# Kernel tuning notes

Hardware: AMD Instinct MI355X
Metric: run time of the kernel (lower is better)

Reference implementation:

```python
import jax, jax.numpy as jnp
import numpy as np
from jax import lax

B, T, H = 128, 8192, 96


def setup_inputs() -> dict:
    key = jax.random.key(0)
    ks = jax.random.split(key, 7)
    s = 1.0 / np.sqrt(H)  # PyTorch LSTM init scale
    return {
        "x": jax.random.normal(ks[0], (B, T, 1), dtype=jnp.float32),
        "w_ih": jax.random.uniform(ks[1], (4 * H, 1), jnp.float32, -s, s),
        "w_hh": jax.random.uniform(ks[2], (4 * H, H), jnp.float32, -s, s),
        "b_ih": jax.random.uniform(ks[3], (4 * H,), jnp.float32, -s, s),
        "b_hh": jax.random.uniform(ks[4], (4 * H,), jnp.float32, -s, s),
        "w_out": jax.random.uniform(ks[5], (1, H), jnp.float32, -s, s),
        "b_out": jax.random.uniform(ks[6], (1,), jnp.float32, -s, s),
    }


def reference(x, w_ih, w_hh, b_ih, b_hh, w_out, b_out):
    # x: [B, T, 1]; single-layer batch_first LSTM, zero initial (h, c).
    Bb, Tt, _ = x.shape
    Hh = w_hh.shape[1]
    # Precompute input contribution to all gates: [T, B, 4H]
    xg = jnp.einsum("bti,gi->btg", x, w_ih) + b_ih + b_hh
    xg = jnp.transpose(xg, (1, 0, 2))

    def step(carry, g):
        h, c = carry
        gates = g + h @ w_hh.T  # [B, 4H]
        i, f, gg, o = jnp.split(gates, 4, axis=-1)  # PyTorch order: i, f, g, o
        i = jax.nn.sigmoid(i)
        f = jax.nn.sigmoid(f)
        gg = jnp.tanh(gg)
        o = jax.nn.sigmoid(o)
        c = f * c + i * gg
        h = o * jnp.tanh(c)
        return (h, c), h

    h0 = jnp.zeros((Bb, Hh), x.dtype)
    (_, _), hs = lax.scan(step, (h0, h0), xg)  # hs: [T, B, H]
    hs = jnp.transpose(hs, (1, 0, 2))  # [B, T, H]
    return hs @ w_out.T + b_out  # [B, T, 1]
```

## Files before the change

### kernel.cpp

```cpp
#include <hip/hip_runtime.h>


#define T_LEN 8192
#define H_DIM 96
#define NTHR  256
#define CHUNK 128
#define LOG2E 1.44269504f

typedef float    f32x4 __attribute__((ext_vector_type(4)));
typedef _Float16 half8 __attribute__((ext_vector_type(8)));

#define MFMA16(A, B, C)                                                        \
    __builtin_amdgcn_mfma_f32_16x16x32_f16(__builtin_bit_cast(half8, (A)),     \
                                           __builtin_bit_cast(half8, (B)),     \
                                           (C), 0, 0, 0)

__device__ __forceinline__ float sig2(float s) {
    return __builtin_amdgcn_rcpf(1.0f + __builtin_amdgcn_exp2f(-s));
}
__device__ __forceinline__ float tanh2(float sg) {
    return 1.0f - 2.0f * __builtin_amdgcn_rcpf(1.0f + __builtin_amdgcn_exp2f(sg));
}

__device__ __forceinline__ f32x4 load_afrag(const float* __restrict__ w_hh,
                                            const float* __restrict__ w_out,
                                            int mt, int kt, int m, int quad) {
    half8 f;
    if (mt < 24) {
        const int r = m & 3;
        const float scale = (r == 2) ? 2.0f * LOG2E : LOG2E;
        const int orig = r * 96 + 4 * mt + (m >> 2);
        const float* src = w_hh + orig * H_DIM + kt * 32 + quad * 8;
        #pragma unroll
        for (int jj = 0; jj < 8; ++jj) f[jj] = (_Float16)(scale * src[jj]);
    } else {
        #pragma unroll
        for (int jj = 0; jj < 8; ++jj)
            f[jj] = (m == 0) ? (_Float16)w_out[kt * 32 + quad * 8 + jj]
                             : (_Float16)0.0f;
    }
    return __builtin_bit_cast(f32x4, f);
}

__global__ __launch_bounds__(NTHR, 2) void lstm_mfma14_kernel(
    const float* __restrict__ x,
    const float* __restrict__ w_ih,
    const float* __restrict__ w_hh,
    const float* __restrict__ b_ih,
    const float* __restrict__ b_hh,
    const float* __restrict__ w_out,
    const float* __restrict__ b_out,
    float* __restrict__ y)
{
    const int tid  = threadIdx.x;
    const int wv   = tid >> 6;
    const int lane = tid & 63;
    const int m    = lane & 15;
    const int quad = lane >> 4;
    const int cc   = m & 7;
    const int bsub = m >> 3;

    __shared__ __align__(16) _Float16 h_s[2][2][H_DIM];
    __shared__ __align__(16) float    y_buf[2][2][CHUNK];
    __shared__ __align__(16) float    x_s[2][T_LEN];

    {
        const float* xpair = x + (size_t)(2 * blockIdx.x) * T_LEN;
        float* xs = &x_s[0][0];
        for (int i = tid * 4; i < 2 * T_LEN; i += NTHR * 4)
            *reinterpret_cast<f32x4*>(&xs[i]) =
                *reinterpret_cast<const f32x4*>(&xpair[i]);
    }

    const int mt0 = 6 * wv;
    f32x4 af00 = load_afrag(w_hh, w_out, mt0 + 0, 0, m, quad);
    f32x4 af01 = load_afrag(w_hh, w_out, mt0 + 0, 1, m, quad);
    f32x4 af02 = load_afrag(w_hh, w_out, mt0 + 0, 2, m, quad);
    f32x4 af10 = load_afrag(w_hh, w_out, mt0 + 1, 0, m, quad);
    f32x4 af11 = load_afrag(w_hh, w_out, mt0 + 1, 1, m, quad);
    f32x4 af12 = load_afrag(w_hh, w_out, mt0 + 1, 2, m, quad);
    f32x4 af20 = load_afrag(w_hh, w_out, mt0 + 2, 0, m, quad);
    f32x4 af21 = load_afrag(w_hh, w_out, mt0 + 2, 1, m, quad);
    f32x4 af22 = load_afrag(w_hh, w_out, mt0 + 2, 2, m, quad);
    f32x4 af30 = load_afrag(w_hh, w_out, mt0 + 3, 0, m, quad);
    f32x4 af31 = load_afrag(w_hh, w_out, mt0 + 3, 1, m, quad);
    f32x4 af32 = load_afrag(w_hh, w_out, mt0 + 3, 2, m, quad);
    f32x4 af40 = load_afrag(w_hh, w_out, mt0 + 4, 0, m, quad);
    f32x4 af41 = load_afrag(w_hh, w_out, mt0 + 4, 1, m, quad);
    f32x4 af42 = load_afrag(w_hh, w_out, mt0 + 4, 2, m, quad);
    f32x4 af50 = load_afrag(w_hh, w_out, mt0 + 5, 0, m, quad);
    f32x4 af51 = load_afrag(w_hh, w_out, mt0 + 5, 1, m, quad);
    f32x4 af52 = load_afrag(w_hh, w_out, mt0 + 5, 2, m, quad);
    f32x4 afy0 = {0.f, 0.f, 0.f, 0.f};
    f32x4 afy1 = {0.f, 0.f, 0.f, 0.f};
    f32x4 afy2 = {0.f, 0.f, 0.f, 0.f};
    if (wv == 3) {
        afy0 = load_afrag(w_hh, w_out, 24, 0, m, quad);
        afy1 = load_afrag(w_hh, w_out, 24, 1, m, quad);
        afy2 = load_afrag(w_hh, w_out, 24, 2, m, quad);
    }
    f32x4 zero4 = {0.f, 0.f, 0.f, 0.f};
    asm volatile("" : "+v"(af00), "+v"(af01), "+v"(af02), "+v"(af10),
                      "+v"(af11), "+v"(af12), "+v"(af20));
    asm volatile("" : "+v"(af21), "+v"(af22), "+v"(af30), "+v"(af31),
                      "+v"(af32), "+v"(af40), "+v"(af41));
    asm volatile("" : "+v"(af42), "+v"(af50), "+v"(af51), "+v"(af52),
                      "+v"(afy0), "+v"(afy1), "+v"(afy2), "+v"(zero4));

    const int sel  = (cc >= 6) ? (cc - 6) : cc;
    const int cell = 24 * wv + 4 * sel + quad;
    const float bias_i = LOG2E * (b_ih[0 * H_DIM + cell] + b_hh[0 * H_DIM + cell]);
    const float bias_f = LOG2E * (b_ih[1 * H_DIM + cell] + b_hh[1 * H_DIM + cell]);
    const float bias_g = 2.0f * LOG2E * (b_ih[2 * H_DIM + cell] + b_hh[2 * H_DIM + cell]);
    const float bias_o = LOG2E * (b_ih[3 * H_DIM + cell] + b_hh[3 * H_DIM + cell]);
    const float wih_i  = LOG2E * w_ih[0 * H_DIM + cell];
    const float wih_f  = LOG2E * w_ih[1 * H_DIM + cell];
    const float wih_g  = 2.0f * LOG2E * w_ih[2 * H_DIM + cell];
    const float wih_o  = LOG2E * w_ih[3 * H_DIM + cell];
    const float bout   = b_out[0];
    float c = 0.f;
    if (tid < 2 * H_DIM) (&h_s[0][0][0])[tid] = (_Float16)0.0f;
    __syncthreads();

    float x_cur_next = x_s[bsub][0];

    for (int it = 0; it <= T_LEN + 1; ++it) {
        const int p = it & 1;

        f32x4 acc0, acc1, acc2, acc3, acc4, acc5, accy;
        const float x_cur = x_cur_next;

        if (it <= T_LEN) {
            const f32x4 b0 = *reinterpret_cast<const f32x4*>(&h_s[p][bsub][quad * 8]);
            const f32x4 b1 = *reinterpret_cast<const f32x4*>(&h_s[p][bsub][32 + quad * 8]);
            const f32x4 b2 = *reinterpret_cast<const f32x4*>(&h_s[p][bsub][64 + quad * 8]);
            x_cur_next = x_s[bsub][(it + 1 < T_LEN) ? (it + 1) : (T_LEN - 1)];

            acc0 = MFMA16(af00, b0, zero4);
            acc1 = MFMA16(af10, b0, zero4);
            acc2 = MFMA16(af20, b0, zero4);
            acc3 = MFMA16(af30, b0, zero4);
            acc4 = MFMA16(af40, b0, zero4);
            acc5 = MFMA16(af50, b0, zero4);
            acc0 = MFMA16(af01, b1, acc0);
            acc1 = MFMA16(af11, b1, acc1);
            acc2 = MFMA16(af21, b1, acc2);
            acc3 = MFMA16(af31, b1, acc3);
            acc4 = MFMA16(af41, b1, acc4);
            acc5 = MFMA16(af51, b1, acc5);
            acc0 = MFMA16(af02, b2, acc0);
            acc1 = MFMA16(af12, b2, acc1);
            acc2 = MFMA16(af22, b2, acc2);
            acc3 = MFMA16(af32, b2, acc3);
            acc4 = MFMA16(af42, b2, acc4);
            acc5 = MFMA16(af52, b2, acc5);
            if (wv == 3) {
                accy = MFMA16(afy0, b0, zero4);
                accy = MFMA16(afy1, b1, accy);
                accy = MFMA16(afy2, b2, accy);
                if (quad == 0 && cc == 0 && it > 0)
                    y_buf[bsub][((it - 1) >> 7) & 1][(it - 1) & (CHUNK - 1)] =
                        accy.x + bout;
            }
        }

        if ((it & (CHUNK - 1)) == 1 && it > 1 && wv < 2 && lane < 32) {
            const int base = it - 1 - CHUNK;
            const int pb = (base >> 7) & 1;
            const f32x4 v =
                *reinterpret_cast<const f32x4*>(&y_buf[wv][pb][lane * 4]);
            float* yrow = y + (size_t)(2 * blockIdx.x + wv) * T_LEN;
            *reinterpret_cast<f32x4*>(&yrow[base + lane * 4]) = v;
        }

        if (it < T_LEN) {
            f32x4 g4 = acc0;
            if (sel == 1) g4 = acc1;
            if (sel == 2) g4 = acc2;
            if (sel == 3) g4 = acc3;
            if (sel == 4) g4 = acc4;
            if (sel == 5) g4 = acc5;
            const float s0 = g4.x + fmaf(x_cur, wih_i, bias_i);
            const float s1 = g4.y + fmaf(x_cur, wih_f, bias_f);
            const float s2 = g4.z + fmaf(x_cur, wih_g, bias_g);
            const float s3 = g4.w + fmaf(x_cur, wih_o, bias_o);
            const float ig = sig2(s0);
            const float fg = sig2(s1);
            const float gg = tanh2(s2);
            const float og = sig2(s3);
            c = fmaf(fg, c, ig * gg);
            const float h = og * tanh2(2.0f * LOG2E * c);
            if (cc < 6) h_s[p ^ 1][bsub][cell] = (_Float16)h;
        }
        __syncthreads();
    }
}

extern "C" void kernel_launch(void* const* d_in, const int* in_sizes, int n_in,
                              void* d_out, int out_size, void* d_ws, size_t ws_size,
                              hipStream_t stream) {
    const float* x     = (const float*)d_in[0];
    const float* w_ih  = (const float*)d_in[1];
    const float* w_hh  = (const float*)d_in[2];
    const float* b_ih  = (const float*)d_in[3];
    const float* b_hh  = (const float*)d_in[4];
    const float* w_out = (const float*)d_in[5];
    const float* b_out = (const float*)d_in[6];
    float* y = (float*)d_out;

    const int NBLK = 64;
    lstm_mfma14_kernel<<<dim3(NBLK), dim3(NTHR), 0, stream>>>(
        x, w_ih, w_hh, b_ih, b_hh, w_out, b_out, y);
}
```

Measured before the change: 3.482 ms.

## Move output projection and y stores to a dedicated fifth wavefront

Adds a fifth wave per block that handles only the w_out projection MFMAs and the periodic global stores of y. The four gate waves no longer carry the extra three MFMAs and store branch on their critical recurrent path. It also pads the x_s rows and splits the preload loop per row. In exchange the block has more threads, every step's barrier must wait for an additional wave, and the extra wave adds register and scheduling pressure.

After: 3.059 ms. -12.2%, faster.

```diff
diff --git a/kernel.cpp b/kernel.cpp
--- a/kernel.cpp
+++ b/kernel.cpp
@@ -3,7 +3,7 @@
 
 #define T_LEN 8192
 #define H_DIM 96
-#define NTHR  256
+#define NTHR  320
 #define CHUNK 128
 #define LOG2E 1.44269504f
 
@@ -42,7 +42,7 @@
     return __builtin_bit_cast(f32x4, f);
 }
 
-__global__ __launch_bounds__(NTHR, 2) void lstm_mfma14_kernel(
+__global__ __launch_bounds__(NTHR, 2) void lstm_mfma15_kernel(
     const float* __restrict__ x,
     const float* __restrict__ w_ih,
     const float* __restrict__ w_hh,
@@ -62,14 +62,16 @@
 
     __shared__ __align__(16) _Float16 h_s[2][2][H_DIM];
     __shared__ __align__(16) float    y_buf[2][2][CHUNK];
-    __shared__ __align__(16) float    x_s[2][T_LEN];
+    __shared__ __align__(16) float    x_s[2][T_LEN + 8];
 
     {
         const float* xpair = x + (size_t)(2 * blockIdx.x) * T_LEN;
-        float* xs = &x_s[0][0];
-        for (int i = tid * 4; i < 2 * T_LEN; i += NTHR * 4)
-            *reinterpret_cast<f32x4*>(&xs[i]) =
+        for (int i = tid * 4; i < T_LEN; i += NTHR * 4) {
+            *reinterpret_cast<f32x4*>(&x_s[0][i]) =
                 *reinterpret_cast<const f32x4*>(&xpair[i]);
+            *reinterpret_cast<f32x4*>(&x_s[1][i]) =
+                *reinterpret_cast<const f32x4*>(&xpair[T_LEN + i]);
+        }
     }
 
     const int mt0 = 6 * wv;
@@ -94,7 +96,7 @@
     f32x4 afy0 = {0.f, 0.f, 0.f, 0.f};
     f32x4 afy1 = {0.f, 0.f, 0.f, 0.f};
     f32x4 afy2 = {0.f, 0.f, 0.f, 0.f};
-    if (wv == 3) {
+    if (wv == 4) {
         afy0 = load_afrag(w_hh, w_out, 24, 0, m, quad);
         afy1 = load_afrag(w_hh, w_out, 24, 1, m, quad);
         afy2 = load_afrag(w_hh, w_out, 24, 2, m, quad);
@@ -108,7 +110,7 @@
                       "+v"(afy0), "+v"(afy1), "+v"(afy2), "+v"(zero4));
 
     const int sel  = (cc >= 6) ? (cc - 6) : cc;
-    const int cell = 24 * wv + 4 * sel + quad;
+    const int cell = (wv < 4) ? (24 * wv + 4 * sel + quad) : 0;
     const float bias_i = LOG2E * (b_ih[0 * H_DIM + cell] + b_hh[0 * H_DIM + cell]);
     const float bias_f = LOG2E * (b_ih[1 * H_DIM + cell] + b_hh[1 * H_DIM + cell]);
     const float bias_g = 2.0f * LOG2E * (b_ih[2 * H_DIM + cell] + b_hh[2 * H_DIM + cell]);
@@ -127,70 +129,73 @@
     for (int it = 0; it <= T_LEN + 1; ++it) {
         const int p = it & 1;
 
-        f32x4 acc0, acc1, acc2, acc3, acc4, acc5, accy;
-        const float x_cur = x_cur_next;
-
-        if (it <= T_LEN) {
-            const f32x4 b0 = *reinterpret_cast<const f32x4*>(&h_s[p][bsub][quad * 8]);
-            const f32x4 b1 = *reinterpret_cast<const f32x4*>(&h_s[p][bsub][32 + quad * 8]);
-            const f32x4 b2 = *reinterpret_cast<const f32x4*>(&h_s[p][bsub][64 + quad * 8]);
-            x_cur_next = x_s[bsub][(it + 1 < T_LEN) ? (it + 1) : (T_LEN - 1)];
-
-            acc0 = MFMA16(af00, b0, zero4);
-            acc1 = MFMA16(af10, b0, zero4);
-            acc2 = MFMA16(af20, b0, zero4);
-            acc3 = MFMA16(af30, b0, zero4);
-            acc4 = MFMA16(af40, b0, zero4);
-            acc5 = MFMA16(af50, b0, zero4);
-            acc0 = MFMA16(af01, b1, acc0);
-            acc1 = MFMA16(af11, b1, acc1);
-            acc2 = MFMA16(af21, b1, acc2);
-            acc3 = MFMA16(af31, b1, acc3);
-            acc4 = MFMA16(af41, b1, acc4);
-            acc5 = MFMA16(af51, b1, acc5);
-            acc0 = MFMA16(af02, b2, acc0);
-            acc1 = MFMA16(af12, b2, acc1);
-            acc2 = MFMA16(af22, b2, acc2);
-            acc3 = MFMA16(af32, b2, acc3);
-            acc4 = MFMA16(af42, b2, acc4);
-            acc5 = MFMA16(af52, b2, acc5);
-            if (wv == 3) {
-                accy = MFMA16(afy0, b0, zero4);
+        if (wv < 4) {
+            if (it < T_LEN) {
+                const f32x4 b0 = *reinterpret_cast<const f32x4*>(&h_s[p][bsub][quad * 8]);
+                const f32x4 b1 = *reinterpret_cast<const f32x4*>(&h_s[p][bsub][32 + quad * 8]);
+                const f32x4 b2 = *reinterpret_cast<const f32x4*>(&h_s[p][bsub][64 + quad * 8]);
+                const float x_cur = x_cur_next;
+                x_cur_next = x_s[bsub][(it + 1 < T_LEN) ? (it + 1) : (T_LEN - 1)];
+
+                f32x4 acc0 = MFMA16(af00, b0, zero4);
+                f32x4 acc1 = MFMA16(af10, b0, zero4);
+                f32x4 acc2 = MFMA16(af20, b0, zero4);
+                f32x4 acc3 = MFMA16(af30, b0, zero4);
+                f32x4 acc4 = MFMA16(af40, b0, zero4);
+                f32x4 acc5 = MFMA16(af50, b0, zero4);
+                acc0 = MFMA16(af01, b1, acc0);
+                acc1 = MFMA16(af11, b1, acc1);
+                acc2 = MFMA16(af21, b1, acc2);
+                acc3 = MFMA16(af31, b1, acc3);
+                acc4 = MFMA16(af41, b1, acc4);
+                acc5 = MFMA16(af51, b1, acc5);
+                acc0 = MFMA16(af02, b2, acc0);
+                acc1 = MFMA16(af12, b2, acc1);
+                acc2 = MFMA16(af22, b2, acc2);
+                acc3 = MFMA16(af32, b2, acc3);
+                acc4 = MFMA16(af42, b2, acc4);
+                acc5 = MFMA16(af52, b2, acc5);
+
+                f32x4 g4 = acc0;
+                if (sel == 1) g4 = acc1;
+                if (sel == 2) g4 = acc2;
+                if (sel == 3) g4 = acc3;
+                if (sel == 4) g4 = acc4;
+                if (sel == 5) g4 = acc5;
+                const float s0 = g4.x + fmaf(x_cur, wih_i, bias_i);
+                const float s1 = g4.y + fmaf(x_cur, wih_f, bias_f);
+                const float s2 = g4.z + fmaf(x_cur, wih_g, bias_g);
+                const float s3 = g4.w + fmaf(x_cur, wih_o, bias_o);
+                const float ig = sig2(s0);
+                const float fg = sig2(s1);
+                const float gg = tanh2(s2);
+                const float og = sig2(s3);
+                c = fmaf(fg, c, ig * gg);
+                const float h = og * tanh2(2.0f * LOG2E * c);
+                if (cc < 6) h_s[p ^ 1][bsub][cell] = (_Float16)h;
+            }
+        } else {
+            if (it <= T_LEN) {
+                const f32x4 b0 = *reinterpret_cast<const f32x4*>(&h_s[p][bsub][quad * 8]);
+                const f32x4 b1 = *reinterpret_cast<const f32x4*>(&h_s[p][bsub][32 + quad * 8]);
+                const f32x4 b2 = *reinterpret_cast<const f32x4*>(&h_s[p][bsub][64 + quad * 8]);
+                f32x4 accy = MFMA16(afy0, b0, zero4);
                 accy = MFMA16(afy1, b1, accy);
                 accy = MFMA16(afy2, b2, accy);
                 if (quad == 0 && cc == 0 && it > 0)
                     y_buf[bsub][((it - 1) >> 7) & 1][(it - 1) & (CHUNK - 1)] =
                         accy.x + bout;
             }
-        }
-
-        if ((it & (CHUNK - 1)) == 1 && it > 1 && wv < 2 && lane < 32) {
-            const int base = it - 1 - CHUNK;
-            const int pb = (base >> 7) & 1;
-            const f32x4 v =
-                *reinterpret_cast<const f32x4*>(&y_buf[wv][pb][lane * 4]);
-            float* yrow = y + (size_t)(2 * blockIdx.x + wv) * T_LEN;
-            *reinterpret_cast<f32x4*>(&yrow[base + lane * 4]) = v;
-        }
-
-        if (it < T_LEN) {
-            f32x4 g4 = acc0;
-            if (sel == 1) g4 = acc1;
-            if (sel == 2) g4 = acc2;
-            if (sel == 3) g4 = acc3;
-            if (sel == 4) g4 = acc4;
-            if (sel == 5) g4 = acc5;
-            const float s0 = g4.x + fmaf(x_cur, wih_i, bias_i);
-            const float s1 = g4.y + fmaf(x_cur, wih_f, bias_f);
-            const float s2 = g4.z + fmaf(x_cur, wih_g, bias_g);
-            const float s3 = g4.w + fmaf(x_cur, wih_o, bias_o);
-            const float ig = sig2(s0);
-            const float fg = sig2(s1);
-            const float gg = tanh2(s2);
-            const float og = sig2(s3);
-            c = fmaf(fg, c, ig * gg);
-            const float h = og * tanh2(2.0f * LOG2E * c);
-            if (cc < 6) h_s[p ^ 1][bsub][cell] = (_Float16)h;
+            if ((it & (CHUNK - 1)) == 1 && it > 1) {
+                const int base = it - 1 - CHUNK;
+                const int pb   = (base >> 7) & 1;
+                const int bsel = lane >> 5;
+                const int li   = lane & 31;
+                const f32x4 v =
+                    *reinterpret_cast<const f32x4*>(&y_buf[bsel][pb][li * 4]);
+                float* yrow = y + (size_t)(2 * blockIdx.x + bsel) * T_LEN;
+                *reinterpret_cast<f32x4*>(&yrow[base + li * 4]) = v;
+            }
         }
         __syncthreads();
     }
@@ -209,6 +214,6 @@
     float* y = (float*)d_out;
 
     const int NBLK = 64;
-    lstm_mfma14_kernel<<<dim3(NBLK), dim3(NTHR), 0, stream>>>(
+    lstm_mfma15_kernel<<<dim3(NBLK), dim3(NTHR), 0, stream>>>(
         x, w_ih, w_hh, b_ih, b_hh, w_out, b_out, y);
 }
```
